# Kernel tuning notes

Hardware: AMD Instinct MI355X
Metric: run time of the kernel (lower is better)

The kernel has to match this reference:

```python
import jax, jax.numpy as jnp
import numpy as np

T = 4096          # tokens (batch*seq)
DIM = 2048        # model dim
INTER = 1024      # moe_inter_dim
E = 32            # n_routed_experts
TOPK = 6          # n_activated_experts
G = 8             # n_expert_groups
TOPK_G = 4        # n_limited_groups
SHARED_INTER = 2 * INTER  # n_shared_experts * moe_inter_dim
ROUTE_SCALE = 1.0


def setup_inputs() -> dict:
    key = jax.random.key(0)
    ks = jax.random.split(key, 8)
    s = 0.02
    return {
        "x": jax.random.normal(ks[0], (T, DIM), jnp.float32),
        "gate_w": jax.random.normal(ks[1], (E, DIM), jnp.float32) * s,
        "wg": jax.random.normal(ks[2], (E, DIM, INTER), jnp.float32) * s,   # gate_proj (stored [in,out])
        "wu": jax.random.normal(ks[3], (E, DIM, INTER), jnp.float32) * s,   # up_proj
        "wd": jax.random.normal(ks[4], (E, INTER, DIM), jnp.float32) * s,   # down_proj
        "swg": jax.random.normal(ks[5], (DIM, SHARED_INTER), jnp.float32) * s,
        "swu": jax.random.normal(ks[6], (DIM, SHARED_INTER), jnp.float32) * s,
        "swd": jax.random.normal(ks[7], (SHARED_INTER, DIM), jnp.float32) * s,
    }


def _gate(x, gate_w):
    # scores = softmax(x @ W^T); bias is None since dim != 7168 -> group score = amax
    scores = jax.nn.softmax(x @ gate_w.T, axis=-1)          # [T, E]
    orig = scores
    gs = scores.reshape(x.shape[0], G, E // G)              # [T, G, E/G]
    group_scores = gs.max(axis=-1)                          # [T, G]
    _, gidx = jax.lax.top_k(group_scores, TOPK_G)           # [T, TOPK_G]
    gmask = jnp.zeros((x.shape[0], G), bool).at[
        jnp.arange(x.shape[0])[:, None], gidx].set(True)
    masked = jnp.where(gmask[:, :, None], gs, -jnp.inf).reshape(x.shape[0], E)
    _, idx = jax.lax.top_k(masked, TOPK)                    # [T, TOPK]
    w = jnp.take_along_axis(orig, idx, axis=1) * ROUTE_SCALE  # softmax path: no renorm
    return w, idx


def reference(x, gate_w, wg, wu, wd, swg, swu, swd):
    weights, indices = _gate(x, gate_w)
    # combine[t, e] = routing weight of expert e for token t (0 if not selected)
    combine = (jax.nn.one_hot(indices, E, dtype=x.dtype) * weights[..., None]).sum(axis=1)  # [T, E]
    y = jnp.zeros_like(x)
    for e in range(E):  # fixed small loop over structurally distinct expert params
        h = jax.nn.silu(x @ wg[e]) * (x @ wu[e])            # [T, INTER]
        y = y + (h @ wd[e]) * combine[:, e:e + 1]
    shared = (jax.nn.silu(x @ swg) * (x @ swu)) @ swd       # shared experts MLP
    return y + shared
```

## Files before the change

### kernel.cpp

```cpp
#include <hip/hip_runtime.h>
#include <hip/hip_bf16.h>

typedef float f32x4 __attribute__((ext_vector_type(4)));
typedef __bf16 bf16x8 __attribute__((ext_vector_type(8)));
typedef unsigned short u16;

#define T_TOK 4096
#define DIMK 2048
#define INTERN 1024
#define NEXP 32
#define NTOPK 6
#define NGRP 8
#define NTOPG 4
#define SINTER 2048
#define MAXPADROWS 29184

__device__ __forceinline__ void glds16(const void* g, void* l) {
    auto* gp = (const __attribute__((address_space(1))) int*)(g);
    auto* lp = (__attribute__((address_space(3))) int*)(l);
    __builtin_amdgcn_global_load_lds(gp, lp, 16, 0, 0);
}

__device__ __forceinline__ size_t toff(int row, int k, int K) {
    int g = (k >> 3) & 7;
    return (size_t)(row >> 7) * (size_t)(128 * K) + (size_t)(k >> 6) * 8192 +
           (size_t)((row & 127) * 64 + ((g ^ (row & 7)) << 3) + (k & 7));
}

__global__ __launch_bounds__(256) void cast_x_tiled_kernel(const float* __restrict__ in, u16* __restrict__ out) {
    int gi = (blockIdx.x * 256 + threadIdx.x) * 8;
    int row = gi >> 11, k = gi & 2047;
    const float4* p = reinterpret_cast<const float4*>(in + gi);
    float4 a = p[0], b = p[1];
    bf16x8 v;
    v[0] = (__bf16)a.x; v[1] = (__bf16)a.y; v[2] = (__bf16)a.z; v[3] = (__bf16)a.w;
    v[4] = (__bf16)b.x; v[5] = (__bf16)b.y; v[6] = (__bf16)b.z; v[7] = (__bf16)b.w;
    *reinterpret_cast<bf16x8*>(out + toff(row, k, DIMK)) = v;
}

template <int KD, int JD>
__global__ __launch_bounds__(256) void trans_tiled_kernel(const float* __restrict__ in, u16* __restrict__ out) {
    __shared__ float tile[64 * 65];
    const int t = threadIdx.x;
    const float* ib = in + (size_t)blockIdx.z * KD * JD;
    u16* ob = out + (size_t)blockIdx.z * KD * JD;
    const int j0 = blockIdx.x * 64, k0 = blockIdx.y * 64;
    {
        const int c4 = (t & 15) * 4;
#pragma unroll
        for (int i = 0; i < 4; ++i) {
            const int r = (t >> 4) + i * 16;
            float4 v = *reinterpret_cast<const float4*>(&ib[(size_t)(k0 + r) * JD + j0 + c4]);
            tile[r * 65 + c4 + 0] = v.x;
            tile[r * 65 + c4 + 1] = v.y;
            tile[r * 65 + c4 + 2] = v.z;
            tile[r * 65 + c4 + 3] = v.w;
        }
    }
    __syncthreads();
    {
        const int jl = t >> 2, kh = (t & 3) * 16;
        const int n = j0 + jl;
        bf16x8 v0, v1;
#pragma unroll
        for (int j = 0; j < 8; ++j) v0[j] = (__bf16)tile[(kh + j) * 65 + jl];
#pragma unroll
        for (int j = 0; j < 8; ++j) v1[j] = (__bf16)tile[(kh + 8 + j) * 65 + jl];
        *reinterpret_cast<bf16x8*>(ob + toff(n, k0 + kh, KD)) = v0;
        *reinterpret_cast<bf16x8*>(ob + toff(n, k0 + kh + 8, KD)) = v1;
    }
}

template <int KD, int JD>
__global__ __launch_bounds__(256) void cat_trans_kernel(const float* __restrict__ g0, const float* __restrict__ u0,
                                                        u16* __restrict__ out) {
    __shared__ float tile[64 * 65];
    const int t = threadIdx.x;
    const size_t so = (size_t)blockIdx.z * KD * JD;
    u16* ob = out + (size_t)blockIdx.z * (2 * (size_t)KD * JD);
    const int j0 = blockIdx.x * 32, k0 = blockIdx.y * 64;
    const int kl = t >> 2, jf = (t & 3) * 4;
#pragma unroll
    for (int s = 0; s < 2; ++s) {
        const float* src = (s ? u0 : g0) + so;
#pragma unroll
        for (int rep = 0; rep < 2; ++rep) {
            int jb = jf + rep * 16;
            float4 v = *reinterpret_cast<const float4*>(&src[(size_t)(k0 + kl) * JD + j0 + jb]);
            int nl = ((jb >> 4) << 5) + s * 16 + (jb & 15);
            tile[kl * 65 + nl + 0] = v.x;
            tile[kl * 65 + nl + 1] = v.y;
            tile[kl * 65 + nl + 2] = v.z;
            tile[kl * 65 + nl + 3] = v.w;
        }
    }
    __syncthreads();
    {
        const int nl = t >> 2, kh = (t & 3) * 16;
        const int n = 2 * j0 + nl;
        bf16x8 v0, v1;
#pragma unroll
        for (int j = 0; j < 8; ++j) v0[j] = (__bf16)tile[(kh + j) * 65 + nl];
#pragma unroll
        for (int j = 0; j < 8; ++j) v1[j] = (__bf16)tile[(kh + 8 + j) * 65 + nl];
        *reinterpret_cast<bf16x8*>(ob + toff(n, k0 + kh, KD)) = v0;
        *reinterpret_cast<bf16x8*>(ob + toff(n, k0 + kh + 8, KD)) = v1;
    }
}

__global__ __launch_bounds__(64) void gate_kernel(const float* __restrict__ x, const float* __restrict__ gw,
                                                  int* __restrict__ counts, int* __restrict__ ids,
                                                  int* __restrict__ tok2row, float* __restrict__ wtok) {
    const int t = blockIdx.x;
    const int lane = threadIdx.x;
    __shared__ float logits[NEXP];
    const float4* xr = reinterpret_cast<const float4*>(x + (size_t)t * DIMK);
    for (int e = 0; e < NEXP; ++e) {
        const float4* gr = reinterpret_cast<const float4*>(gw + (size_t)e * DIMK);
        float acc = 0.f;
#pragma unroll
        for (int i = 0; i < DIMK / 4 / 64; ++i) {
            float4 xv = xr[lane + i * 64];
            float4 gv = gr[lane + i * 64];
            acc += xv.x * gv.x + xv.y * gv.y + xv.z * gv.z + xv.w * gv.w;
        }
#pragma unroll
        for (int s = 32; s; s >>= 1) acc += __shfl_xor(acc, s);
        if (lane == 0) logits[e] = acc;
    }
    if (lane != 0) return;
    float sc[NEXP];
#pragma unroll
    for (int e = 0; e < NEXP; ++e) sc[e] = logits[e];
    float mx = sc[0];
#pragma unroll
    for (int e = 1; e < NEXP; ++e) mx = fmaxf(mx, sc[e]);
    float ssum = 0.f;
#pragma unroll
    for (int e = 0; e < NEXP; ++e) { sc[e] = __expf(sc[e] - mx); ssum += sc[e]; }
    const float inv = 1.f / ssum;
    float gsc[NGRP];
#pragma unroll
    for (int g = 0; g < NGRP; ++g) {
        float m2 = sc[g * 4];
#pragma unroll
        for (int j = 1; j < 4; ++j) m2 = fmaxf(m2, sc[g * 4 + j]);
        gsc[g] = m2;
    }
    int gsel = 0;
    for (int r = 0; r < NTOPG; ++r) {
        float bv = -1.f; int bi = 0;
#pragma unroll
        for (int g = 0; g < NGRP; ++g) {
            bool c = (((gsel >> g) & 1) == 0) && (gsc[g] > bv);
            bv = c ? gsc[g] : bv; bi = c ? g : bi;
        }
        gsel |= (1 << bi);
    }
    float msk[NEXP];
#pragma unroll
    for (int e = 0; e < NEXP; ++e) msk[e] = ((gsel >> (e >> 2)) & 1) ? sc[e] : -1.f;
    for (int r = 0; r < NTOPK; ++r) {
        float bv = -3.f; int bi = 0;
#pragma unroll
        for (int e = 0; e < NEXP; ++e) {
            bool c = msk[e] > bv;
            bv = c ? msk[e] : bv; bi = c ? e : bi;
        }
#pragma unroll
        for (int e = 0; e < NEXP; ++e) if (e == bi) msk[e] = -2.f;
        float w = bv * inv;
        int slot = atomicAdd(&counts[bi], 1);
        ids[bi * T_TOK + slot] = t;
        tok2row[t * NTOPK + r] = (bi << 12) | slot;
        wtok[t * NTOPK + r] = w;
    }
}

__global__ void scan_kernel(const int* __restrict__ counts, int* __restrict__ poff) {
    if (threadIdx.x == 0) {
        int o = 0;
        for (int e = 0; e < NEXP; ++e) { poff[e] = o; o += (counts[e] + 127) & ~127; }
    }
}


__global__ __launch_bounds__(512, 2) void gemm1_fused_kernel(
    const u16* __restrict__ xbT, const u16* __restrict__ WcatE, u16* __restrict__ H,
    const u16* __restrict__ WcatS, u16* __restrict__ Hs,
    const int* __restrict__ counts, const int* __restrict__ poff, const int* __restrict__ ids) {
    __shared__ u16 Alds[2 * 16384];
    __shared__ u16 Blds[2 * 16384];
    constexpr int NT = DIMK / 64;

    int bm, bn, M, Mpad, hbase, HKdim, e = 0;
    const u16* b0;
    u16* ho;
    bool gath;
    if (blockIdx.z < 32) {
        int lin = blockIdx.x + 16 * (blockIdx.y + 8 * blockIdx.z);
        e = 31 - (((lin >> 10) << 3) | (lin & 7));
        int j = (lin >> 3) & 127;
        bm = j & 15; bn = j >> 4;
        M = counts[e];
        if (bm * 256 >= M) return;
        Mpad = (M + 127) & ~127;
        hbase = poff[e];
        b0 = WcatE + (size_t)e * 2048 * DIMK;
        ho = H; HKdim = INTERN; gath = true;
    } else {
        int lin = blockIdx.x + 16 * (blockIdx.y + 8 * (blockIdx.z - 32));
        int swz = (lin & 7) * 32 + (lin >> 3);
        bm = swz & 15; bn = swz >> 4;
        M = T_TOK; Mpad = T_TOK; hbase = 0;
        b0 = WcatS; ho = Hs; HKdim = SINTER; gath = false;
    }

    const int tid = threadIdx.x;
    const int t8 = tid * 8;
    size_t aSrc[2][2];
#pragma unroll
    for (int h = 0; h < 2; ++h)
#pragma unroll
        for (int j = 0; j < 2; ++j) {
            int drow = j * 64 + (tid >> 3);
            int row = bm * 256 + h * 128 + drow;
            int tok;
            if (gath) { int cr = row < M ? row : M - 1; tok = ids[e * T_TOK + cr]; }
            else tok = row;
            int slot = (tid & 7) ^ (drow & 7) ^ (tok & 7);
            aSrc[h][j] = (size_t)(tok >> 7) * (size_t)(128 * 2048) + (size_t)((tok & 127) * 64 + slot * 8);
        }
    const u16* bCh[2] = { b0 + (size_t)(2 * bn + 0) * (128 * 2048), b0 + (size_t)(2 * bn + 1) * (128 * 2048) };

    const int lane = tid & 63, wv = tid >> 6;
    const int wr = wv >> 2, wc = wv & 3;
    const int l15 = lane & 15, lk = lane >> 4;

    f32x4 acc[8][4];
#pragma unroll
    for (int m = 0; m < 8; ++m)
#pragma unroll
        for (int n = 0; n < 4; ++n) acc[m][n] = {0.f, 0.f, 0.f, 0.f};

    auto SA = [&](int kt, int h, int buf) {
        glds16(xbT + aSrc[h][0] + (size_t)kt * 8192, &Alds[buf * 16384 + h * 8192 + t8]);
        glds16(xbT + aSrc[h][1] + (size_t)kt * 8192, &Alds[buf * 16384 + h * 8192 + 4096 + t8]);
    };
    auto SB = [&](int kt, int h, int buf) {
        glds16(bCh[h] + (size_t)kt * 8192 + t8, &Blds[buf * 16384 + h * 8192 + t8]);
        glds16(bCh[h] + (size_t)kt * 8192 + 4096 + t8, &Blds[buf * 16384 + h * 8192 + 4096 + t8]);
    };
    bf16x8 afr[4][2], bfr0[2][2], bfr1[2][2];
    auto DSRA = [&](int buf, int mh) {
#pragma unroll
        for (int mi = 0; mi < 4; ++mi)
#pragma unroll
            for (int ki = 0; ki < 2; ++ki) {
                int rl = wr * 128 + mh * 64 + mi * 16 + l15;
                int g = ki * 4 + lk;
                afr[mi][ki] = *reinterpret_cast<const bf16x8*>(
                    &Alds[buf * 16384 + (rl >> 7) * 8192 + (rl & 127) * 64 + ((g ^ (rl & 7)) << 3)]);
            }
    };
    auto DSRB = [&](int buf, int nh, bf16x8 (&bf)[2][2]) {
#pragma unroll
        for (int nj = 0; nj < 2; ++nj)
#pragma unroll
            for (int ki = 0; ki < 2; ++ki) {
                int rc = wc * 64 + (nh * 2 + nj) * 16 + l15;
                int g = ki * 4 + lk;
                bf[nj][ki] = *reinterpret_cast<const bf16x8*>(
                    &Blds[buf * 16384 + (rc >> 7) * 8192 + (rc & 127) * 64 + ((g ^ (rc & 7)) << 3)]);
            }
    };

    SA(0, 0, 0); SA(0, 1, 0); SB(0, 0, 0); SB(0, 1, 0); SA(1, 0, 1);
    asm volatile("s_waitcnt vmcnt(2)" ::: "memory");
    __builtin_amdgcn_s_barrier();

#pragma unroll 1
    for (int t = 0; t < NT; ++t) {
        const int buf = t & 1;
        DSRA(buf, 0);
        DSRB(buf, 0, bfr0);
        if (t + 1 < NT) SA(t + 1, 1, buf ^ 1);
        __builtin_amdgcn_s_barrier();
        __builtin_amdgcn_s_setprio(1);
#pragma unroll
        for (int ki = 0; ki < 2; ++ki)
#pragma unroll
            for (int mi = 0; mi < 4; ++mi)
#pragma unroll
                for (int nj = 0; nj < 2; ++nj)
                    acc[mi][nj] = __builtin_amdgcn_mfma_f32_16x16x32_bf16(afr[mi][ki], bfr0[nj][ki], acc[mi][nj], 0, 0, 0);
        __builtin_amdgcn_s_setprio(0);
        __builtin_amdgcn_s_barrier();
        DSRB(buf, 1, bfr1);
        if (t + 1 < NT) SB(t + 1, 0, buf ^ 1);
        __builtin_amdgcn_s_barrier();
        __builtin_amdgcn_s_setprio(1);
#pragma unroll
        for (int ki = 0; ki < 2; ++ki)
#pragma unroll
            for (int mi = 0; mi < 4; ++mi)
#pragma unroll
                for (int nj = 0; nj < 2; ++nj)
                    acc[mi][2 + nj] = __builtin_amdgcn_mfma_f32_16x16x32_bf16(afr[mi][ki], bfr1[nj][ki], acc[mi][2 + nj], 0, 0, 0);
        __builtin_amdgcn_s_setprio(0);
        __builtin_amdgcn_s_barrier();
        DSRA(buf, 1);
        if (t + 1 < NT) SB(t + 1, 1, buf ^ 1);
        __builtin_amdgcn_s_barrier();
        __builtin_amdgcn_s_setprio(1);
#pragma unroll
        for (int ki = 0; ki < 2; ++ki)
#pragma unroll
            for (int mi = 0; mi < 4; ++mi)
#pragma unroll
                for (int nj = 0; nj < 2; ++nj)
                    acc[4 + mi][2 + nj] = __builtin_amdgcn_mfma_f32_16x16x32_bf16(afr[mi][ki], bfr1[nj][ki], acc[4 + mi][2 + nj], 0, 0, 0);
        __builtin_amdgcn_s_setprio(0);
        __builtin_amdgcn_s_barrier();
        if (t + 2 < NT) SA(t + 2, 0, buf);
        __builtin_amdgcn_s_setprio(1);
#pragma unroll
        for (int ki = 0; ki < 2; ++ki)
#pragma unroll
            for (int mi = 0; mi < 4; ++mi)
#pragma unroll
                for (int nj = 0; nj < 2; ++nj)
                    acc[4 + mi][nj] = __builtin_amdgcn_mfma_f32_16x16x32_bf16(afr[mi][ki], bfr0[nj][ki], acc[4 + mi][nj], 0, 0, 0);
        __builtin_amdgcn_s_setprio(0);
        if (t + 2 < NT) { asm volatile("s_waitcnt vmcnt(2)" ::: "memory"); }
        else { asm volatile("s_waitcnt vmcnt(0)" ::: "memory"); }
        __builtin_amdgcn_s_barrier();
    }

#pragma unroll
    for (int mI = 0; mI < 8; ++mI) {
#pragma unroll
        for (int r = 0; r < 4; ++r) {
            int grow = bm * 256 + wr * 128 + mI * 16 + lk * 4 + r;
            if (grow < Mpad) {
#pragma unroll
                for (int nh = 0; nh < 2; ++nh) {
                    float gg = acc[mI][nh * 2 + 0][r];
                    float uu = acc[mI][nh * 2 + 1][r];
                    float h = gg / (1.f + __expf(-gg)) * uu;
                    int n = bn * 256 + wc * 64 + nh * 32 + l15;
                    int jcol = ((n >> 5) << 4) + (n & 15);
                    __bf16 hb = (__bf16)h;
                    ho[toff(hbase + grow, jcol, HKdim)] = __builtin_bit_cast(u16, hb);
                }
            }
        }
    }
}

__global__ __launch_bounds__(512, 2) void gemm2_fused_kernel(
    const u16* __restrict__ H, const u16* __restrict__ wdT, u16* __restrict__ Ye,
    const u16* __restrict__ Hs, const u16* __restrict__ swdT, u16* __restrict__ Yss,
    const int* __restrict__ counts, const int* __restrict__ poff) {
    __shared__ u16 Alds[2 * 16384];
    __shared__ u16 Blds[2 * 16384];
    constexpr int NT = 16;

    int bm, bn, M, rowbase, AKK, kt0;
    const u16 *aBase, *bBase;
    u16* yo;
    if (blockIdx.z < 32) {
        int lin = blockIdx.x + 16 * (blockIdx.y + 8 * blockIdx.z);
        int e = 31 - (((lin >> 10) << 3) | (lin & 7));
        int j = (lin >> 3) & 127;
        bm = j & 15; bn = j >> 4;
        M = counts[e];
        if (bm * 256 >= M) return;
        rowbase = poff[e];
        aBase = H + (size_t)poff[e] * INTERN;
        bBase = wdT + (size_t)e * 2048 * INTERN;
        yo = Ye; AKK = INTERN; kt0 = 0;
    } else {
        int lin = blockIdx.x + 16 * (blockIdx.y + 8 * (blockIdx.z - 32));
        int swz = (lin & 7) * 32 + (lin >> 3);
        bm = swz & 15; bn = (swz >> 4) & 7;
        int ks = swz >> 7;
        M = T_TOK; rowbase = ks * T_TOK;
        aBase = Hs; bBase = swdT; yo = Yss; AKK = SINTER; kt0 = ks * 16;
    }
    const u16* aCh[2] = { aBase + (size_t)(2 * bm + 0) * (size_t)(128 * AKK) + (size_t)kt0 * 8192,
                          aBase + (size_t)(2 * bm + 1) * (size_t)(128 * AKK) + (size_t)kt0 * 8192 };
    const u16* bCh[2] = { bBase + (size_t)(2 * bn + 0) * (size_t)(128 * AKK) + (size_t)kt0 * 8192,
                          bBase + (size_t)(2 * bn + 1) * (size_t)(128 * AKK) + (size_t)kt0 * 8192 };
    const int tid = threadIdx.x;
    const int t8 = tid * 8;
    const int lane = tid & 63, wv = tid >> 6;
    const int wr = wv >> 2, wc = wv & 3;
    const int l15 = lane & 15, lk = lane >> 4;

    f32x4 acc[8][4];
#pragma unroll
    for (int m = 0; m < 8; ++m)
#pragma unroll
        for (int n = 0; n < 4; ++n) acc[m][n] = {0.f, 0.f, 0.f, 0.f};

    auto SA = [&](int kt, int h, int buf) {
        glds16(aCh[h] + (size_t)kt * 8192 + t8, &Alds[buf * 16384 + h * 8192 + t8]);
        glds16(aCh[h] + (size_t)kt * 8192 + 4096 + t8, &Alds[buf * 16384 + h * 8192 + 4096 + t8]);
    };
    auto SB = [&](int kt, int h, int buf) {
        glds16(bCh[h] + (size_t)kt * 8192 + t8, &Blds[buf * 16384 + h * 8192 + t8]);
        glds16(bCh[h] + (size_t)kt * 8192 + 4096 + t8, &Blds[buf * 16384 + h * 8192 + 4096 + t8]);
    };
    bf16x8 afr[4][2], bfr0[2][2], bfr1[2][2];
    auto DSRA = [&](int buf, int mh) {
#pragma unroll
        for (int mi = 0; mi < 4; ++mi)
#pragma unroll
            for (int ki = 0; ki < 2; ++ki) {
                int rl = wr * 128 + mh * 64 + mi * 16 + l15;
                int g = ki * 4 + lk;
                afr[mi][ki] = *reinterpret_cast<const bf16x8*>(
                    &Alds[buf * 16384 + (rl >> 7) * 8192 + (rl & 127) * 64 + ((g ^ (rl & 7)) << 3)]);
            }
    };
    auto DSRB = [&](int buf, int nh, bf16x8 (&bf)[2][2]) {
#pragma unroll
        for (int nj = 0; nj < 2; ++nj)
#pragma unroll
            for (int ki = 0; ki < 2; ++ki) {
                int rc = wc * 64 + (nh * 2 + nj) * 16 + l15;
                int g = ki * 4 + lk;
                bf[nj][ki] = *reinterpret_cast<const bf16x8*>(
                    &Blds[buf * 16384 + (rc >> 7) * 8192 + (rc & 127) * 64 + ((g ^ (rc & 7)) << 3)]);
            }
    };

    SA(0, 0, 0); SA(0, 1, 0); SB(0, 0, 0); SB(0, 1, 0); SA(1, 0, 1);
    asm volatile("s_waitcnt vmcnt(2)" ::: "memory");
    __builtin_amdgcn_s_barrier();

#pragma unroll 1
    for (int t = 0; t < NT; ++t) {
        const int buf = t & 1;
        DSRA(buf, 0);
        DSRB(buf, 0, bfr0);
        if (t + 1 < NT) SA(t + 1, 1, buf ^ 1);
        __builtin_amdgcn_s_barrier();
        __builtin_amdgcn_s_setprio(1);
#pragma unroll
        for (int ki = 0; ki < 2; ++ki)
#pragma unroll
            for (int mi = 0; mi < 4; ++mi)
#pragma unroll
                for (int nj = 0; nj < 2; ++nj)
                    acc[mi][nj] = __builtin_amdgcn_mfma_f32_16x16x32_bf16(afr[mi][ki], bfr0[nj][ki], acc[mi][nj], 0, 0, 0);
        __builtin_amdgcn_s_setprio(0);
        __builtin_amdgcn_s_barrier();
        DSRB(buf, 1, bfr1);
        if (t + 1 < NT) SB(t + 1, 0, buf ^ 1);
        __builtin_amdgcn_s_barrier();
        __builtin_amdgcn_s_setprio(1);
#pragma unroll
        for (int ki = 0; ki < 2; ++ki)
#pragma unroll
            for (int mi = 0; mi < 4; ++mi)
#pragma unroll
                for (int nj = 0; nj < 2; ++nj)
                    acc[mi][2 + nj] = __builtin_amdgcn_mfma_f32_16x16x32_bf16(afr[mi][ki], bfr1[nj][ki], acc[mi][2 + nj], 0, 0, 0);
        __builtin_amdgcn_s_setprio(0);
        __builtin_amdgcn_s_barrier();
        DSRA(buf, 1);
        if (t + 1 < NT) SB(t + 1, 1, buf ^ 1);
        __builtin_amdgcn_s_barrier();
        __builtin_amdgcn_s_setprio(1);
#pragma unroll
        for (int ki = 0; ki < 2; ++ki)
#pragma unroll
            for (int mi = 0; mi < 4; ++mi)
#pragma unroll
                for (int nj = 0; nj < 2; ++nj)
                    acc[4 + mi][2 + nj] = __builtin_amdgcn_mfma_f32_16x16x32_bf16(afr[mi][ki], bfr1[nj][ki], acc[4 + mi][2 + nj], 0, 0, 0);
        __builtin_amdgcn_s_setprio(0);
        __builtin_amdgcn_s_barrier();
        if (t + 2 < NT) SA(t + 2, 0, buf);
        __builtin_amdgcn_s_setprio(1);
#pragma unroll
        for (int ki = 0; ki < 2; ++ki)
#pragma unroll
            for (int mi = 0; mi < 4; ++mi)
#pragma unroll
                for (int nj = 0; nj < 2; ++nj)
                    acc[4 + mi][nj] = __builtin_amdgcn_mfma_f32_16x16x32_bf16(afr[mi][ki], bfr0[nj][ki], acc[4 + mi][nj], 0, 0, 0);
        __builtin_amdgcn_s_setprio(0);
        if (t + 2 < NT) { asm volatile("s_waitcnt vmcnt(2)" ::: "memory"); }
        else { asm volatile("s_waitcnt vmcnt(0)" ::: "memory"); }
        __builtin_amdgcn_s_barrier();
    }

#pragma unroll
    for (int mI = 0; mI < 8; ++mI) {
#pragma unroll
        for (int r = 0; r < 4; ++r) {
            int grow = bm * 256 + wr * 128 + mI * 16 + lk * 4 + r;
            if (grow < M) {
                u16* yr = yo + (size_t)(rowbase + grow) * 2048;
#pragma unroll
                for (int ni = 0; ni < 4; ++ni) {
                    int col = bn * 256 + wc * 64 + ni * 16 + l15;
                    __bf16 yb = (__bf16)acc[mI][ni][r];
                    yr[col] = __builtin_bit_cast(u16, yb);
                }
            }
        }
    }
}

__global__ __launch_bounds__(256) void combine_kernel(const u16* __restrict__ Yss, const u16* __restrict__ Ye,
                                                      const int* __restrict__ tok2row, const float* __restrict__ wtok,
                                                      const int* __restrict__ poff, float* __restrict__ out) {
    const int t = blockIdx.x;
    const int c = threadIdx.x * 8;
    bf16x8 v0 = *reinterpret_cast<const bf16x8*>(Yss + (size_t)t * 2048 + c);
    bf16x8 v1 = *reinterpret_cast<const bf16x8*>(Yss + (size_t)(T_TOK + t) * 2048 + c);
    float acc[8];
#pragma unroll
    for (int j = 0; j < 8; ++j) acc[j] = (float)v0[j] + (float)v1[j];
#pragma unroll
    for (int r = 0; r < NTOPK; ++r) {
        int pk = tok2row[t * NTOPK + r];
        int e = pk >> 12, sl = pk & 4095;
        int row = poff[e] + sl;
        float w = wtok[t * NTOPK + r];
        bf16x8 v = *reinterpret_cast<const bf16x8*>(Ye + (size_t)row * 2048 + c);
#pragma unroll
        for (int j = 0; j < 8; ++j) acc[j] += w * (float)v[j];
    }
    float4 o0 = {acc[0], acc[1], acc[2], acc[3]};
    float4 o1 = {acc[4], acc[5], acc[6], acc[7]};
    float4* po = reinterpret_cast<float4*>(out + (size_t)t * 2048 + c);
    po[0] = o0; po[1] = o1;
}

extern "C" void kernel_launch(void* const* d_in, const int* in_sizes, int n_in,
                              void* d_out, int out_size, void* d_ws, size_t ws_size,
                              hipStream_t stream) {
    const float* x = (const float*)d_in[0];
    const float* gate_w = (const float*)d_in[1];
    const float* wg = (const float*)d_in[2];
    const float* wu = (const float*)d_in[3];
    const float* wd = (const float*)d_in[4];
    const float* swg = (const float*)d_in[5];
    const float* swu = (const float*)d_in[6];
    const float* swd = (const float*)d_in[7];
    float* out = (float*)d_out;

    char* ws = (char*)d_ws;
    size_t off = 0;
    auto alloc = [&](size_t bytes) {
        void* p = ws + off;
        off = (off + bytes + 255) & ~(size_t)255;
        return p;
    };
    u16* xbT = (u16*)alloc((size_t)T_TOK * DIMK * 2);
    u16* H = (u16*)alloc((size_t)MAXPADROWS * INTERN * 2);
    u16* Hs = (u16*)alloc((size_t)T_TOK * SINTER * 2);
    u16* Ye = (u16*)alloc((size_t)MAXPADROWS * 2048 * 2);
    u16* Yss = (u16*)alloc((size_t)2 * T_TOK * 2048 * 2);
    int* ids = (int*)alloc((size_t)NEXP * T_TOK * 4);
    int* tok2row = (int*)alloc((size_t)T_TOK * NTOPK * 4);
    float* wtok = (float*)alloc((size_t)T_TOK * NTOPK * 4);
    int* counts = (int*)alloc(NEXP * 4);
    int* poff = (int*)alloc(NEXP * 4);
    u16* WcatS = (u16*)alloc((size_t)(2 * SINTER) * DIMK * 2);
    u16* swdT = (u16*)alloc((size_t)DIMK * SINTER * 2);
    u16* WcatE = (u16*)alloc((size_t)NEXP * (2 * INTERN) * DIMK * 2);
    u16* wdT = WcatE;

    hipMemsetAsync(counts, 0, NEXP * 4, stream);
    cast_x_tiled_kernel<<<(T_TOK * DIMK) / (256 * 8), 256, 0, stream>>>(x, xbT);
    gate_kernel<<<T_TOK, 64, 0, stream>>>(x, gate_w, counts, ids, tok2row, wtok);
    scan_kernel<<<1, 64, 0, stream>>>(counts, poff);

    cat_trans_kernel<DIMK, SINTER><<<dim3(SINTER / 32, DIMK / 64, 1), 256, 0, stream>>>(swg, swu, WcatS);
    cat_trans_kernel<DIMK, INTERN><<<dim3(INTERN / 32, DIMK / 64, NEXP), 256, 0, stream>>>(wg, wu, WcatE);
    trans_tiled_kernel<SINTER, DIMK><<<dim3(DIMK / 64, SINTER / 64, 1), 256, 0, stream>>>(swd, swdT);

    gemm1_fused_kernel<<<dim3(16, 8, 34), 512, 0, stream>>>(
        xbT, WcatE, H, WcatS, Hs, counts, poff, ids);

    trans_tiled_kernel<INTERN, DIMK><<<dim3(DIMK / 64, INTERN / 64, NEXP), 256, 0, stream>>>(wd, wdT);

    gemm2_fused_kernel<<<dim3(16, 8, 34), 512, 0, stream>>>(
        H, wdT, Ye, Hs, swdT, Yss, counts, poff);

    combine_kernel<<<T_TOK, 256, 0, stream>>>(Yss, Ye, tok2row, wtok, poff, out);
}
```

Baseline: 1.034 ms.

## Triple-buffer B tiles in LDS and prefetch weights two K-steps ahead

Both fused GEMM kernels now keep three LDS buffers for the weight (B) tiles instead of two. B loads are issued two K-iterations ahead, while both halves of the next A tile are loaded at the start of each iteration. The vmcnt waits are adjusted so only the newest B prefetch may remain in flight. This aims to hide more global-load latency on the weight stream, at the cost of 160KB of LDS per block. That is the full CU LDS, so at most one block fits per CU and the launch-bounds hint of two is unreachable.

```diff
diff --git a/kernel.cpp b/kernel.cpp
--- a/kernel.cpp
+++ b/kernel.cpp
@@ -190,7 +190,7 @@
     const u16* __restrict__ WcatS, u16* __restrict__ Hs,
     const int* __restrict__ counts, const int* __restrict__ poff, const int* __restrict__ ids) {
     __shared__ u16 Alds[2 * 16384];
-    __shared__ u16 Blds[2 * 16384];
+    __shared__ u16 Blds[3 * 16384];
     constexpr int NT = DIMK / 64;
 
     int bm, bn, M, Mpad, hbase, HKdim, e = 0;
@@ -275,16 +275,20 @@
             }
     };
 
-    SA(0, 0, 0); SA(0, 1, 0); SB(0, 0, 0); SB(0, 1, 0); SA(1, 0, 1);
-    asm volatile("s_waitcnt vmcnt(2)" ::: "memory");
+    SA(0, 0, 0); SA(0, 1, 0);
+    SB(0, 0, 0); SB(0, 1, 0);
+    SB(1, 0, 1); SB(1, 1, 1);
+    asm volatile("s_waitcnt vmcnt(4)" ::: "memory");
     __builtin_amdgcn_s_barrier();
 
 #pragma unroll 1
     for (int t = 0; t < NT; ++t) {
-        const int buf = t & 1;
-        DSRA(buf, 0);
-        DSRB(buf, 0, bfr0);
-        if (t + 1 < NT) SA(t + 1, 1, buf ^ 1);
+        const int abuf = t & 1;
+        const int bbuf = t % 3;
+        const int b3 = (t + 2) % 3;
+        DSRA(abuf, 0);
+        DSRB(bbuf, 0, bfr0);
+        if (t + 1 < NT) { SA(t + 1, 0, abuf ^ 1); SA(t + 1, 1, abuf ^ 1); }
         __builtin_amdgcn_s_barrier();
         __builtin_amdgcn_s_setprio(1);
 #pragma unroll
@@ -296,8 +300,8 @@
                     acc[mi][nj] = __builtin_amdgcn_mfma_f32_16x16x32_bf16(afr[mi][ki], bfr0[nj][ki], acc[mi][nj], 0, 0, 0);
         __builtin_amdgcn_s_setprio(0);
         __builtin_amdgcn_s_barrier();
-        DSRB(buf, 1, bfr1);
-        if (t + 1 < NT) SB(t + 1, 0, buf ^ 1);
+        DSRB(bbuf, 1, bfr1);
+        if (t + 2 < NT) SB(t + 2, 0, b3);
         __builtin_amdgcn_s_barrier();
         __builtin_amdgcn_s_setprio(1);
 #pragma unroll
@@ -309,8 +313,8 @@
                     acc[mi][2 + nj] = __builtin_amdgcn_mfma_f32_16x16x32_bf16(afr[mi][ki], bfr1[nj][ki], acc[mi][2 + nj], 0, 0, 0);
         __builtin_amdgcn_s_setprio(0);
         __builtin_amdgcn_s_barrier();
-        DSRA(buf, 1);
-        if (t + 1 < NT) SB(t + 1, 1, buf ^ 1);
+        DSRA(abuf, 1);
+        if (t + 2 < NT) SB(t + 2, 1, b3);
         __builtin_amdgcn_s_barrier();
         __builtin_amdgcn_s_setprio(1);
 #pragma unroll
@@ -322,7 +326,6 @@
                     acc[4 + mi][2 + nj] = __builtin_amdgcn_mfma_f32_16x16x32_bf16(afr[mi][ki], bfr1[nj][ki], acc[4 + mi][2 + nj], 0, 0, 0);
         __builtin_amdgcn_s_setprio(0);
         __builtin_amdgcn_s_barrier();
-        if (t + 2 < NT) SA(t + 2, 0, buf);
         __builtin_amdgcn_s_setprio(1);
 #pragma unroll
         for (int ki = 0; ki < 2; ++ki)
@@ -332,7 +335,7 @@
                 for (int nj = 0; nj < 2; ++nj)
                     acc[4 + mi][nj] = __builtin_amdgcn_mfma_f32_16x16x32_bf16(afr[mi][ki], bfr0[nj][ki], acc[4 + mi][nj], 0, 0, 0);
         __builtin_amdgcn_s_setprio(0);
-        if (t + 2 < NT) { asm volatile("s_waitcnt vmcnt(2)" ::: "memory"); }
+        if (t + 2 < NT) { asm volatile("s_waitcnt vmcnt(4)" ::: "memory"); }
         else { asm volatile("s_waitcnt vmcnt(0)" ::: "memory"); }
         __builtin_amdgcn_s_barrier();
     }
@@ -363,7 +366,7 @@
     const u16* __restrict__ Hs, const u16* __restrict__ swdT, u16* __restrict__ Yss,
     const int* __restrict__ counts, const int* __restrict__ poff) {
     __shared__ u16 Alds[2 * 16384];
-    __shared__ u16 Blds[2 * 16384];
+    __shared__ u16 Blds[3 * 16384];
     constexpr int NT = 16;
 
     int bm, bn, M, rowbase, AKK, kt0;
@@ -436,16 +439,20 @@
             }
     };
 
-    SA(0, 0, 0); SA(0, 1, 0); SB(0, 0, 0); SB(0, 1, 0); SA(1, 0, 1);
-    asm volatile("s_waitcnt vmcnt(2)" ::: "memory");
+    SA(0, 0, 0); SA(0, 1, 0);
+    SB(0, 0, 0); SB(0, 1, 0);
+    SB(1, 0, 1); SB(1, 1, 1);
+    asm volatile("s_waitcnt vmcnt(4)" ::: "memory");
     __builtin_amdgcn_s_barrier();
 
 #pragma unroll 1
     for (int t = 0; t < NT; ++t) {
-        const int buf = t & 1;
-        DSRA(buf, 0);
-        DSRB(buf, 0, bfr0);
-        if (t + 1 < NT) SA(t + 1, 1, buf ^ 1);
+        const int abuf = t & 1;
+        const int bbuf = t % 3;
+        const int b3 = (t + 2) % 3;
+        DSRA(abuf, 0);
+        DSRB(bbuf, 0, bfr0);
+        if (t + 1 < NT) { SA(t + 1, 0, abuf ^ 1); SA(t + 1, 1, abuf ^ 1); }
         __builtin_amdgcn_s_barrier();
         __builtin_amdgcn_s_setprio(1);
 #pragma unroll
@@ -457,8 +464,8 @@
                     acc[mi][nj] = __builtin_amdgcn_mfma_f32_16x16x32_bf16(afr[mi][ki], bfr0[nj][ki], acc[mi][nj], 0, 0, 0);
         __builtin_amdgcn_s_setprio(0);
         __builtin_amdgcn_s_barrier();
-        DSRB(buf, 1, bfr1);
-        if (t + 1 < NT) SB(t + 1, 0, buf ^ 1);
+        DSRB(bbuf, 1, bfr1);
+        if (t + 2 < NT) SB(t + 2, 0, b3);
         __builtin_amdgcn_s_barrier();
         __builtin_amdgcn_s_setprio(1);
 #pragma unroll
@@ -470,8 +477,8 @@
                     acc[mi][2 + nj] = __builtin_amdgcn_mfma_f32_16x16x32_bf16(afr[mi][ki], bfr1[nj][ki], acc[mi][2 + nj], 0, 0, 0);
         __builtin_amdgcn_s_setprio(0);
         __builtin_amdgcn_s_barrier();
-        DSRA(buf, 1);
-        if (t + 1 < NT) SB(t + 1, 1, buf ^ 1);
+        DSRA(abuf, 1);
+        if (t + 2 < NT) SB(t + 2, 1, b3);
         __builtin_amdgcn_s_barrier();
         __builtin_amdgcn_s_setprio(1);
 #pragma unroll
@@ -483,7 +490,6 @@
                     acc[4 + mi][2 + nj] = __builtin_amdgcn_mfma_f32_16x16x32_bf16(afr[mi][ki], bfr1[nj][ki], acc[4 + mi][2 + nj], 0, 0, 0);
         __builtin_amdgcn_s_setprio(0);
         __builtin_amdgcn_s_barrier();
-        if (t + 2 < NT) SA(t + 2, 0, buf);
         __builtin_amdgcn_s_setprio(1);
 #pragma unroll
         for (int ki = 0; ki < 2; ++ki)
@@ -493,7 +499,7 @@
                 for (int nj = 0; nj < 2; ++nj)
                     acc[4 + mi][nj] = __builtin_amdgcn_mfma_f32_16x16x32_bf16(afr[mi][ki], bfr0[nj][ki], acc[4 + mi][nj], 0, 0, 0);
         __builtin_amdgcn_s_setprio(0);
-        if (t + 2 < NT) { asm volatile("s_waitcnt vmcnt(2)" ::: "memory"); }
+        if (t + 2 < NT) { asm volatile("s_waitcnt vmcnt(4)" ::: "memory"); }
         else { asm volatile("s_waitcnt vmcnt(0)" ::: "memory"); }
         __builtin_amdgcn_s_barrier();
     }
```

Result: faster. 1.006 ms (-2.7%).
